# Kernel optimization log

Hardware: AMD Instinct MI355X
Metric: run time of the kernel (lower is better)

## Reference

```python
import jax, jax.numpy as jnp
import numpy as np

B, S, D, H = 4, 4096, 1024, 64

def setup_inputs() -> dict:
    key = jax.random.key(0)
    k1, k2, k3, k4 = jax.random.split(key, 4)
    inp = {
        'input': jax.random.normal(k1, (B, S, D), dtype=jnp.float32),
        'Wq': jax.random.normal(k2, (D, H), dtype=jnp.float32) * (D ** -0.5),
        'Wk': jax.random.normal(k3, (D, H), dtype=jnp.float32) * (D ** -0.5),
        'Wv': jax.random.normal(k4, (D, H), dtype=jnp.float32) * (D ** -0.5),
    }
    return inp

def reference(input, Wq, Wk, Wv):
    # Projections: [B,S,D] @ [D,H] -> [B,S,H]
    q = input @ Wq
    k = input @ Wk
    v = input @ Wv
    head_size = Wq.shape[-1]
    # Scaled scores: [B,S,S]
    scores = jnp.einsum('bqh,bkh->bqk', q, k) * (head_size ** -0.5)
    seq_len = input.shape[1]
    causal = jnp.tril(jnp.ones((seq_len, seq_len), dtype=bool))
    masked = jnp.where(causal, scores, -jnp.inf)
    weights = jax.nn.softmax(masked, axis=-1)
    # dropout p=0.0 -> identity
    return jnp.einsum('bqk,bkh->bqh', weights, v)
```

## Files before the change

kernel.cpp:

```cpp
#include <hip/hip_runtime.h>

#define NS 8

typedef __attribute__((ext_vector_type(8))) short sh8;
typedef __attribute__((ext_vector_type(4))) short sh4;
typedef __attribute__((ext_vector_type(4))) float f4;

#define QSCALE 0.18033688011112042f

typedef const __attribute__((address_space(1))) unsigned int* gas_t;
typedef __attribute__((address_space(3))) unsigned int* las_t;
#define GLD16(g, l) __builtin_amdgcn_global_load_lds((gas_t)(g), (las_t)(l), 16, 0, 0)

static __device__ __forceinline__ unsigned short f2bf(float f) {
  unsigned u = __builtin_bit_cast(unsigned, f);
  u += 0x7fffu + ((u >> 16) & 1u);
  return (unsigned short)(u >> 16);
}
static __device__ __forceinline__ float bf2f(unsigned short s) {
  unsigned u = ((unsigned)s) << 16;
  return __builtin_bit_cast(float, u);
}

__global__ __launch_bounds__(256) void wt_kernel(const float* __restrict__ Wq,
                                                 const float* __restrict__ Wk,
                                                 const float* __restrict__ Wv,
                                                 unsigned short* __restrict__ Wt2) {
  int blk = blockIdx.x;
  int band = blk >> 3;
  int widx = band >> 2;
  const float* W = widx == 0 ? Wq : (widx == 1 ? Wk : Wv);
  int ncol = (band & 3) * 16;
  int t = threadIdx.x;
  int kt = (blk & 7) * 4 + (t >> 6);
  int lane = t & 63, q = lane >> 4, l15 = lane & 15;
  const float* src = W + (size_t)(kt * 32 + q * 8) * 64 + ncol + l15;
  sh8 o;
#pragma unroll
  for (int j = 0; j < 8; ++j) o[j] = (short)f2bf(src[(size_t)j * 64]);
  *(sh8*)&Wt2[((size_t)(band * 32 + kt) * 64 + lane) * 8] = o;
}

__global__ __launch_bounds__(256, 8) void proj_kernel(const float* __restrict__ in,
                                                      const unsigned short* __restrict__ Wt2,
                                                      unsigned short* __restrict__ Qg,
                                                      unsigned short* __restrict__ Kg,
                                                      unsigned short* __restrict__ Vtg) {
  __shared__ __align__(16) char lds[8192];
  int t = threadIdx.x;
  int w = t >> 6, lane = t & 63, q = lane >> 4, l15 = lane & 15;
  int m0 = blockIdx.x * 16;

  const float* ga = in + (size_t)(m0 + l15) * 1024 + q * 8 + (w & 1) * 4;
  const unsigned short* gb = Wt2 + (size_t)(w * 3) * 16384 + lane * 8;

  f4 acc[3];
  f4 z = {0.f, 0.f, 0.f, 0.f};
#pragma unroll
  for (int nt = 0; nt < 3; ++nt) acc[nt] = z;

#define STAGE(kt, buf)                                                        \
  { if (w < 2) GLD16(ga + (kt) * 32, lds + (buf) * 2048 + w * 1024); }

  STAGE(0, 0);
  for (int kt = 0; kt < 32; ++kt) {
    int cur = kt & 1;
    __syncthreads();
    if (kt + 1 < 32) STAGE(kt + 1, cur ^ 1);

    sh8 bfr[3];
#pragma unroll
    for (int nt = 0; nt < 3; ++nt)
      bfr[nt] = *(const sh8*)(gb + nt * 16384 + kt * 512);

    const f4* Af = (const f4*)(lds + cur * 2048);
    f4 lo = Af[lane], hi = Af[64 + lane];
    sh8 a;
#pragma unroll
    for (int j = 0; j < 4; ++j) {
      a[j] = (short)f2bf(lo[j]);
      a[4 + j] = (short)f2bf(hi[j]);
    }
#pragma unroll
    for (int nt = 0; nt < 3; ++nt)
      acc[nt] = __builtin_amdgcn_mfma_f32_16x16x32_bf16(a, bfr[nt], acc[nt], 0, 0, 0);
  }
#undef STAGE

  __syncthreads();
  float* vred = (float*)lds;
#pragma unroll
  for (int nt = 0; nt < 3; ++nt) {
    int band = w * 3 + nt;
#pragma unroll
    for (int r = 0; r < 4; ++r) {
      int row = q * 4 + r;
      float v = acc[nt][r];
      if (band < 4) {
        Qg[(size_t)(m0 + row) * 64 + band * 16 + l15] = f2bf(v * QSCALE);
      } else if (band < 8) {
        Kg[(size_t)(m0 + row) * 64 + (band - 4) * 16 + l15] = f2bf(v);
      } else {
        vred[row * 69 + (band - 8) * 16 + l15] = v;
      }
    }
  }
  __syncthreads();
  {
    int h = t >> 2, sl = (t & 3) * 4;
    int bb = m0 >> 12, s0 = m0 & 4095;
    sh4 vv;
#pragma unroll
    for (int j = 0; j < 4; ++j) vv[j] = (short)f2bf(vred[(sl + j) * 69 + h]);
    *(sh4*)&Vtg[(((size_t)(bb * 64 + h)) << 12) + s0 + sl] = vv;
  }
}

__global__ __launch_bounds__(256, 4) void attn_split(const unsigned short* __restrict__ Qg,
                                                     const unsigned short* __restrict__ Kg,
                                                     const unsigned short* __restrict__ Vtg,
                                                     unsigned short* __restrict__ Opart,
                                                     float* __restrict__ Lpart) {
  __shared__ unsigned short Ks[64 * 72];
  __shared__ unsigned short Vs[64 * 72];
  __shared__ unsigned short Pw[4 * 16 * 72];
  int t = threadIdx.x;
  int b = blockIdx.y;
  int qt = 63 - (int)(blockIdx.x >> 3);
  int sp = blockIdx.x & 7;
  int wave = t >> 6, lane = t & 63, quad = lane >> 4, l15 = lane & 15;
  unsigned short* Pws = Pw + wave * 16 * 72;

  int qrow0 = qt * 64 + wave * 16;
  size_t pbase = ((size_t)sp * 4 + b) * 4096;

  int nkt = qt + 1;
  int chunk = (nkt + NS - 1) / NS;
  int t0 = sp * chunk, t1 = min(nkt, t0 + chunk);
  if (t0 >= t1) {
#pragma unroll
    for (int r = 0; r < 4; ++r) {
      size_t row = pbase + qrow0 + quad * 4 + r;
#pragma unroll
      for (int ht = 0; ht < 4; ++ht) Opart[row * 64 + ht * 16 + l15] = 0;
      if (l15 == 0) Lpart[row] = 0.f;
    }
    return;
  }

  sh8 qa[2];
#pragma unroll
  for (int ks = 0; ks < 2; ++ks)
    qa[ks] = *(const sh8*)&Qg[(size_t)((b << 12) + qrow0 + l15) * 64 + ks * 32 + quad * 8];

  sh8 ones;
#pragma unroll
  for (int j = 0; j < 8; ++j) ones[j] = (short)0x3F80;

  f4 o[5];
  f4 z = {0.f, 0.f, 0.f, 0.f};
#pragma unroll
  for (int ht = 0; ht < 5; ++ht) o[ht] = z;

  int r0 = t >> 3, o0 = (t & 7) * 8;
  int r1 = (t + 256) >> 3, o1 = ((t + 256) & 7) * 8;
  const unsigned short* kg0 = Kg + (size_t)((b << 12) + r0) * 64 + o0;
  const unsigned short* kg1 = Kg + (size_t)((b << 12) + r1) * 64 + o1;
  const unsigned short* vg0 = Vtg + (((size_t)(b * 64 + r0)) << 12) + o0;
  const unsigned short* vg1 = Vtg + (((size_t)(b * 64 + r1)) << 12) + o1;

  sh8 kr0, kr1, vr0, vr1;
  {
    size_t ko = (size_t)t0 * 64 * 64;
    kr0 = *(const sh8*)(kg0 + ko); kr1 = *(const sh8*)(kg1 + ko);
    vr0 = *(const sh8*)(vg0 + t0 * 64); vr1 = *(const sh8*)(vg1 + t0 * 64);
  }

  for (int kt = t0; kt < t1; ++kt) {
    __syncthreads();
    *(sh8*)&Ks[r0 * 72 + o0] = kr0;
    *(sh8*)&Ks[r1 * 72 + o1] = kr1;
    *(sh8*)&Vs[r0 * 72 + o0] = vr0;
    *(sh8*)&Vs[r1 * 72 + o1] = vr1;
    if (kt + 1 < t1) {
      size_t ko = (size_t)(kt + 1) * 64 * 64;
      kr0 = *(const sh8*)(kg0 + ko); kr1 = *(const sh8*)(kg1 + ko);
      vr0 = *(const sh8*)(vg0 + (kt + 1) * 64); vr1 = *(const sh8*)(vg1 + (kt + 1) * 64);
    }
    __syncthreads();

    f4 st[4];
#pragma unroll
    for (int nt = 0; nt < 4; ++nt) st[nt] = z;
#pragma unroll
    for (int ks = 0; ks < 2; ++ks) {
#pragma unroll
      for (int nt = 0; nt < 4; ++nt) {
        sh8 kb = *(const sh8*)&Ks[(nt * 16 + l15) * 72 + ks * 32 + quad * 8];
        st[nt] = __builtin_amdgcn_mfma_f32_16x16x32_bf16(kb, qa[ks], st[nt], 0, 0, 0);
      }
    }

    if (kt == nkt - 1) {
      int qrow = qrow0 + l15;
#pragma unroll
      for (int nt = 0; nt < 4; ++nt) {
        int key0 = kt * 64 + nt * 16 + quad * 4;
#pragma unroll
        for (int r = 0; r < 4; ++r)
          if (key0 + r > qrow) st[nt][r] = -__builtin_inff();
      }
    }

#pragma unroll
    for (int nt = 0; nt < 4; ++nt) {
      sh4 pk;
#pragma unroll
      for (int r = 0; r < 4; ++r) pk[r] = (short)f2bf(exp2f(st[nt][r]));
      *(sh4*)&Pws[l15 * 72 + nt * 16 + quad * 4] = pk;
    }
    asm volatile("s_waitcnt lgkmcnt(0)" ::: "memory");

#pragma unroll
    for (int ks = 0; ks < 2; ++ks) {
      sh8 pa = *(const sh8*)&Pws[l15 * 72 + ks * 32 + quad * 8];
#pragma unroll
      for (int ht = 0; ht < 4; ++ht) {
        sh8 vb = *(const sh8*)&Vs[(ht * 16 + l15) * 72 + ks * 32 + quad * 8];
        o[ht] = __builtin_amdgcn_mfma_f32_16x16x32_bf16(pa, vb, o[ht], 0, 0, 0);
      }
      o[4] = __builtin_amdgcn_mfma_f32_16x16x32_bf16(pa, ones, o[4], 0, 0, 0);
    }
  }

#pragma unroll
  for (int r = 0; r < 4; ++r) {
    size_t row = pbase + qrow0 + quad * 4 + r;
#pragma unroll
    for (int ht = 0; ht < 4; ++ht)
      Opart[row * 64 + ht * 16 + l15] = f2bf(o[ht][r]);
    if (l15 == 0) Lpart[row] = o[4][r];
  }
}

__global__ __launch_bounds__(256) void attn_combine(const unsigned short* __restrict__ Opart,
                                                    const float* __restrict__ Lpart,
                                                    float* __restrict__ out) {
  int t = threadIdx.x;
  int r = blockIdx.x * 32 + (t >> 3);
  int h0 = (t & 7) * 8;
  float L = 0.f;
  float acc[8];
#pragma unroll
  for (int j = 0; j < 8; ++j) acc[j] = 0.f;
#pragma unroll
  for (int s = 0; s < NS; ++s) {
    L += Lpart[(size_t)s * 16384 + r];
    sh8 v = *(const sh8*)&Opart[((size_t)s * 16384 + r) * 64 + h0];
#pragma unroll
    for (int j = 0; j < 8; ++j) acc[j] += bf2f((unsigned short)v[j]);
  }
  float inv = 1.f / L;
  f4 o0, o1;
#pragma unroll
  for (int j = 0; j < 4; ++j) { o0[j] = acc[j] * inv; o1[j] = acc[4 + j] * inv; }
  *(f4*)&out[(size_t)r * 64 + h0] = o0;
  *(f4*)&out[(size_t)r * 64 + h0 + 4] = o1;
}

extern "C" void kernel_launch(void* const* d_in, const int* in_sizes, int n_in,
                              void* d_out, int out_size, void* d_ws, size_t ws_size,
                              hipStream_t stream) {
  const float* in = (const float*)d_in[0];
  const float* Wq = (const float*)d_in[1];
  const float* Wk = (const float*)d_in[2];
  const float* Wv = (const float*)d_in[3];
  float* out = (float*)d_out;

  char* ws = (char*)d_ws;
  unsigned short* Wt2   = (unsigned short*)ws;
  unsigned short* Qg    = (unsigned short*)(ws + 393216);
  unsigned short* Kg    = (unsigned short*)(ws + 2490368);
  unsigned short* Vtg   = (unsigned short*)(ws + 4587520);
  unsigned short* Opart = (unsigned short*)(ws + 6684672);
  float*          Lpart = (float*)(ws + 23461888);

  hipLaunchKernelGGL(wt_kernel, dim3(96), dim3(256), 0, stream, Wq, Wk, Wv, Wt2);
  hipLaunchKernelGGL(proj_kernel, dim3(1024), dim3(256), 0, stream, in, Wt2, Qg, Kg, Vtg);
  hipLaunchKernelGGL(attn_split, dim3(64 * NS, 4), dim3(256), 0, stream,
                     Qg, Kg, Vtg, Opart, Lpart);
  hipLaunchKernelGGL(attn_combine, dim3(512), dim3(256), 0, stream,
                     Opart, Lpart, out);
}
```

Baseline: 156.4 us.

## Double proj tile rows, stage weights through LDS with deeper K stages

The projection kernel now computes 32 rows per block instead of 16, so each weight fragment is reused across two M sub-tiles. Both input and weight tiles are loaded into LDS with direct global-to-LDS loads, four K-steps per stage, in a 128KB double buffer. This replaces the per-iteration global weight reads and cuts the number of synchronisation points. The cost is that the large LDS footprint allows only one block per CU, so there are fewer resident waves to hide memory latency. The grid is halved to match.

```diff
diff --git a/kernel.cpp b/kernel.cpp
--- a/kernel.cpp
+++ b/kernel.cpp
@@ -41,78 +41,99 @@
   *(sh8*)&Wt2[((size_t)(band * 32 + kt) * 64 + lane) * 8] = o;
 }
 
-__global__ __launch_bounds__(256, 8) void proj_kernel(const float* __restrict__ in,
+__global__ __launch_bounds__(256, 1) void proj_kernel(const float* __restrict__ in,
                                                       const unsigned short* __restrict__ Wt2,
                                                       unsigned short* __restrict__ Qg,
                                                       unsigned short* __restrict__ Kg,
                                                       unsigned short* __restrict__ Vtg) {
-  __shared__ __align__(16) char lds[8192];
+  __shared__ __align__(16) char lds[131072];
   int t = threadIdx.x;
   int w = t >> 6, lane = t & 63, q = lane >> 4, l15 = lane & 15;
-  int m0 = blockIdx.x * 16;
-
-  const float* ga = in + (size_t)(m0 + l15) * 1024 + q * 8 + (w & 1) * 4;
+  int m0 = blockIdx.x * 32;
+
+  const float* ga = in + (size_t)(m0 + (w >> 1) * 16 + l15) * 1024 + q * 8 + (w & 1) * 4;
   const unsigned short* gb = Wt2 + (size_t)(w * 3) * 16384 + lane * 8;
 
-  f4 acc[3];
+  f4 acc[2][3];
   f4 z = {0.f, 0.f, 0.f, 0.f};
 #pragma unroll
-  for (int nt = 0; nt < 3; ++nt) acc[nt] = z;
-
-#define STAGE(kt, buf)                                                        \
-  { if (w < 2) GLD16(ga + (kt) * 32, lds + (buf) * 2048 + w * 1024); }
+  for (int mt = 0; mt < 2; ++mt)
+#pragma unroll
+    for (int nt = 0; nt < 3; ++nt) acc[mt][nt] = z;
+
+#define STAGE(s, buf)                                                         \
+  {                                                                           \
+    char* base = lds + (buf) * 65536;                                         \
+    const float* gas = ga + (s) * 128;                                        \
+    _Pragma("unroll")                                                         \
+    for (int kk = 0; kk < 4; ++kk) {                                          \
+      GLD16(gas + kk * 32, base + kk * 4096 + w * 1024);                      \
+      _Pragma("unroll")                                                       \
+      for (int nt = 0; nt < 3; ++nt)                                          \
+        GLD16(gb + nt * 16384 + ((s) * 4 + kk) * 512,                         \
+              base + 16384 + (kk * 12 + w * 3 + nt) * 1024);                  \
+    }                                                                         \
+  }
 
   STAGE(0, 0);
-  for (int kt = 0; kt < 32; ++kt) {
-    int cur = kt & 1;
+  for (int s = 0; s < 8; ++s) {
+    int cur = s & 1;
     __syncthreads();
-    if (kt + 1 < 32) STAGE(kt + 1, cur ^ 1);
-
-    sh8 bfr[3];
-#pragma unroll
-    for (int nt = 0; nt < 3; ++nt)
-      bfr[nt] = *(const sh8*)(gb + nt * 16384 + kt * 512);
-
-    const f4* Af = (const f4*)(lds + cur * 2048);
-    f4 lo = Af[lane], hi = Af[64 + lane];
-    sh8 a;
-#pragma unroll
-    for (int j = 0; j < 4; ++j) {
-      a[j] = (short)f2bf(lo[j]);
-      a[4 + j] = (short)f2bf(hi[j]);
-    }
-#pragma unroll
-    for (int nt = 0; nt < 3; ++nt)
-      acc[nt] = __builtin_amdgcn_mfma_f32_16x16x32_bf16(a, bfr[nt], acc[nt], 0, 0, 0);
+    if (s + 1 < 8) STAGE(s + 1, cur ^ 1);
+
+    const f4* Af = (const f4*)(lds + cur * 65536);
+    const sh8* Bf = (const sh8*)(lds + cur * 65536 + 16384);
+#pragma unroll
+    for (int kk = 0; kk < 4; ++kk) {
+      sh8 bfr[3];
+#pragma unroll
+      for (int nt = 0; nt < 3; ++nt)
+        bfr[nt] = Bf[(kk * 12 + w * 3 + nt) * 64 + lane];
+#pragma unroll
+      for (int mt = 0; mt < 2; ++mt) {
+        f4 lo = Af[kk * 256 + mt * 128 + lane];
+        f4 hi = Af[kk * 256 + mt * 128 + 64 + lane];
+        sh8 a;
+#pragma unroll
+        for (int j = 0; j < 4; ++j) {
+          a[j] = (short)f2bf(lo[j]);
+          a[4 + j] = (short)f2bf(hi[j]);
+        }
+#pragma unroll
+        for (int nt = 0; nt < 3; ++nt)
+          acc[mt][nt] = __builtin_amdgcn_mfma_f32_16x16x32_bf16(a, bfr[nt], acc[mt][nt], 0, 0, 0);
+      }
+    }
   }
 #undef STAGE
 
-  __syncthreads();
   float* vred = (float*)lds;
 #pragma unroll
   for (int nt = 0; nt < 3; ++nt) {
     int band = w * 3 + nt;
 #pragma unroll
-    for (int r = 0; r < 4; ++r) {
-      int row = q * 4 + r;
-      float v = acc[nt][r];
-      if (band < 4) {
-        Qg[(size_t)(m0 + row) * 64 + band * 16 + l15] = f2bf(v * QSCALE);
-      } else if (band < 8) {
-        Kg[(size_t)(m0 + row) * 64 + (band - 4) * 16 + l15] = f2bf(v);
-      } else {
-        vred[row * 69 + (band - 8) * 16 + l15] = v;
-      }
-    }
+    for (int mt = 0; mt < 2; ++mt)
+#pragma unroll
+      for (int r = 0; r < 4; ++r) {
+        int row = mt * 16 + q * 4 + r;
+        float v = acc[mt][nt][r];
+        if (band < 4) {
+          Qg[(size_t)(m0 + row) * 64 + band * 16 + l15] = f2bf(v * QSCALE);
+        } else if (band < 8) {
+          Kg[(size_t)(m0 + row) * 64 + (band - 4) * 16 + l15] = f2bf(v);
+        } else {
+          vred[row * 69 + (band - 8) * 16 + l15] = v;
+        }
+      }
   }
   __syncthreads();
   {
-    int h = t >> 2, sl = (t & 3) * 4;
+    int h = t >> 2, sl = (t & 3) * 8;
     int bb = m0 >> 12, s0 = m0 & 4095;
-    sh4 vv;
-#pragma unroll
-    for (int j = 0; j < 4; ++j) vv[j] = (short)f2bf(vred[(sl + j) * 69 + h]);
-    *(sh4*)&Vtg[(((size_t)(bb * 64 + h)) << 12) + s0 + sl] = vv;
+    sh8 vv;
+#pragma unroll
+    for (int j = 0; j < 8; ++j) vv[j] = (short)f2bf(vred[(sl + j) * 69 + h]);
+    *(sh8*)&Vtg[(((size_t)(bb * 64 + h)) << 12) + s0 + sl] = vv;
   }
 }
 
@@ -286,7 +307,7 @@
   float*          Lpart = (float*)(ws + 23461888);
 
   hipLaunchKernelGGL(wt_kernel, dim3(96), dim3(256), 0, stream, Wq, Wk, Wv, Wt2);
-  hipLaunchKernelGGL(proj_kernel, dim3(1024), dim3(256), 0, stream, in, Wt2, Qg, Kg, Vtg);
+  hipLaunchKernelGGL(proj_kernel, dim3(512), dim3(256), 0, stream, in, Wt2, Qg, Kg, Vtg);
   hipLaunchKernelGGL(attn_split, dim3(64 * NS, 4), dim3(256), 0, stream,
                      Qg, Kg, Vtg, Opart, Lpart);
   hipLaunchKernelGGL(attn_combine, dim3(512), dim3(256), 0, stream,
```

Result: faster. 150.1 us (-4.0%).
